# Kernel optimization log

Hardware: AMD Instinct MI355X
Metric: run time of the kernel (lower is better)

The kernel has to match this reference:

```python
import jax, jax.numpy as jnp
import numpy as np

IN_C = 1
BASE_C = 16
N3, N2, N1 = 262144, 65536, 16384

def _quadconv(feat, neigh, w, b):
    # feat: [N, C]; neigh: [N, 9] with -1 padding -> gather via extra zero row
    N = feat.shape[0]
    feat_p = jnp.concatenate([feat, jnp.zeros((1, feat.shape[1]), feat.dtype)], axis=0)
    gidx = jnp.where(neigh == -1, N, neigh)
    col = feat_p[gidx].reshape(N, -1)  # [N, 9*C] im2col
    return col @ w.T + b

def _parent_idx(keys, parent_keys):
    return jnp.searchsorted(parent_keys, keys >> 2)

def _quadpool(feat, keys, parent_keys):
    pidx = _parent_idx(keys, parent_keys)
    p = jax.ops.segment_max(feat, pidx, num_segments=parent_keys.shape[0])
    # original inits with -1e9 and zeroes untouched slots; segment_max uses -inf fill
    return jnp.where(jnp.isneginf(p), jnp.zeros((), feat.dtype), p), pidx

def _quadunpool(feat, keys, parent_keys):
    return feat[_parent_idx(keys, parent_keys)]

def _lin(key, out_f, in_f, scale=0.05):
    kw, kb = jax.random.split(key)
    return (jax.random.normal(kw, (out_f, in_f), jnp.float32) * scale,
            jnp.zeros((out_f,), jnp.float32))

def setup_inputs() -> dict:
    key = jax.random.key(0)
    ks = jax.random.split(key, 12)
    inp = {
        'features': jax.random.normal(ks[0], (N3, IN_C), jnp.float32),
        'keys3': jnp.arange(N3, dtype=jnp.int32),
        'keys2': jnp.arange(N2, dtype=jnp.int32),
        'keys1': jnp.arange(N1, dtype=jnp.int32),
        'neighs3': jax.random.randint(ks[1], (N3, 9), -1, N3, jnp.int32),
        'neighs2': jax.random.randint(ks[2], (N2, 9), -1, N2, jnp.int32),
        'neighs1': jax.random.randint(ks[3], (N1, 9), -1, N1, jnp.int32),
    }
    c = BASE_C
    inp['w_enc1'], inp['b_enc1'] = _lin(ks[4], c, 9 * IN_C)
    inp['w_enc2'], inp['b_enc2'] = _lin(ks[5], 2 * c, 9 * c)
    inp['w_enc3'], inp['b_enc3'] = _lin(ks[6], 4 * c, 9 * 2 * c)
    inp['w_dec1'], inp['b_dec1'] = _lin(ks[7], 2 * c, 9 * 4 * c)
    inp['w_dec2'], inp['b_dec2'] = _lin(ks[8], c, 9 * 2 * c)
    inp['w_head'], inp['b_head'] = _lin(ks[9], IN_C, 9 * c)
    return inp

def reference(features, keys3, keys2, keys1, neighs3, neighs2, neighs1,
              w_enc1, b_enc1, w_enc2, b_enc2, w_enc3, b_enc3,
              w_dec1, b_dec1, w_dec2, b_dec2, w_head, b_head):
    relu = jax.nn.relu
    x8 = relu(_quadconv(features, neighs3, w_enc1, b_enc1))
    x7_p, _ = _quadpool(x8, keys3, keys2)
    x7 = relu(_quadconv(x7_p, neighs2, w_enc2, b_enc2))
    x6_p, _ = _quadpool(x7, keys2, keys1)
    x6 = relu(_quadconv(x6_p, neighs1, w_enc3, b_enc3))
    x7_up = _quadunpool(x6, keys2, keys1)
    x7_dec = relu(_quadconv(x7_up, neighs2, w_dec1, b_dec1))
    x8_up = _quadunpool(x7_dec, keys3, keys2)
    x8_dec = relu(_quadconv(x8_up, neighs3, w_dec2, b_dec2))
    return _quadconv(x8_dec, neighs3, w_head, b_head)
```

## Files before the change

kernel.cpp:

```cpp
#include <hip/hip_runtime.h>
#include <stdint.h>

#define NN3 262144
#define NN2 65536
#define NN1 16384

typedef __attribute__((ext_vector_type(8))) __bf16 bf16x8;
typedef __attribute__((ext_vector_type(4))) float floatx4;

static __device__ __forceinline__ float bf2f(unsigned short u) {
    union { unsigned int i; float f; } v; v.i = ((unsigned int)u) << 16; return v.f;
}
static __device__ __forceinline__ unsigned short f2bf(float f) {
    union { float f; unsigned int i; } v; v.f = f;
    unsigned int x = v.i;
    return (unsigned short)((x + 0x7fffu + ((x >> 16) & 1u)) >> 16);
}
static __device__ __forceinline__ bf16x8 zero_bf16x8() {
    bf16x8 z;
#pragma unroll
    for (int i = 0; i < 8; ++i) z[i] = (__bf16)0.0f;
    return z;
}

__global__ __launch_bounds__(256) void enc1pool_kernel(
    const float* __restrict__ feat, const int* __restrict__ neigh,
    const float* __restrict__ w, const float* __restrict__ b,
    unsigned short* __restrict__ x7p,
    const float* __restrict__ w_enc2, const float* __restrict__ w_enc3,
    const float* __restrict__ w_dec1, const float* __restrict__ w_dec2,
    unsigned short* __restrict__ wb_enc2, unsigned short* __restrict__ wb_enc3,
    unsigned short* __restrict__ wb_dec1, unsigned short* __restrict__ wb_dec2)
{
    {
        int g = blockIdx.x * 256 + threadIdx.x;
        if (g < 4608) wb_enc2[g] = f2bf(w_enc2[g]);
        else {
            g -= 4608;
            if (g < 18432) wb_enc3[g] = f2bf(w_enc3[g]);
            else {
                g -= 18432;
                if (g < 18432) wb_dec1[g] = f2bf(w_dec1[g]);
                else { g -= 18432; if (g < 4608) wb_dec2[g] = f2bf(w_dec2[g]); }
            }
        }
    }
    __shared__ float ws[144];
    __shared__ float bs[16];
    __shared__ int nsh[2304];
    int t = threadIdx.x;
    if (t < 144) ws[t] = w[t];
    if (t < 16)  bs[t] = b[t];
    int base = blockIdx.x * 256;
    for (int e = t; e < 2304; e += 256)
        nsh[e] = __builtin_nontemporal_load(&neigh[(size_t)base * 9 + e]);
    __syncthreads();
    float f[9];
#pragma unroll
    for (int k = 0; k < 9; ++k) { int j = nsh[t * 9 + k]; f[k] = (j < 0) ? 0.0f : feat[j]; }
    float v[16];
#pragma unroll
    for (int co = 0; co < 16; ++co) {
        float a = bs[co];
#pragma unroll
        for (int k = 0; k < 9; ++k) a += f[k] * ws[co * 9 + k];
        v[co] = fmaxf(a, 0.0f);
    }
#pragma unroll
    for (int co = 0; co < 16; ++co) {
        v[co] = fmaxf(v[co], __shfl_xor(v[co], 1));
        v[co] = fmaxf(v[co], __shfl_xor(v[co], 2));
    }
    if ((t & 3) == 0) {
        unsigned int ov[8];
#pragma unroll
        for (int h = 0; h < 8; ++h)
            ov[h] = (unsigned int)f2bf(v[2 * h]) | (((unsigned int)f2bf(v[2 * h + 1])) << 16);
        uint4* dst = (uint4*)(x7p + (size_t)((base + t) >> 2) * 16);
        dst[0] = make_uint4(ov[0], ov[1], ov[2], ov[3]);
        dst[1] = make_uint4(ov[4], ov[5], ov[6], ov[7]);
    }
}

template <int CIN, int COUT, bool SHIFT, bool POOL, int TILES>
__global__ __launch_bounds__(256) void conv_mfma(
    const unsigned short* __restrict__ src, const int* __restrict__ neigh,
    const unsigned short* __restrict__ wb, const float* __restrict__ bias,
    unsigned short* __restrict__ dst)
{
    constexpr int K  = 9 * CIN;
    constexpr int KT = (K + 31) / 32;
    constexpr int NT = COUT / 16;
    __shared__ int nsh[576 * TILES];
    int t = threadIdx.x;
    int rowbase = blockIdx.x * (64 * TILES);
    for (int e = t; e < 576 * TILES; e += 256) {
        int j = __builtin_nontemporal_load(&neigh[(size_t)rowbase * 9 + e]);
        if (SHIFT) j = (j < 0) ? -1 : (j >> 2);
        nsh[e] = j;
    }
    __syncthreads();
    int lane = t & 63;
    int wave = t >> 6;
    int m    = lane & 15;
    int quad = lane >> 4;
    int mrow9 = (wave * 16 + m) * 9;
    floatx4 acc[TILES][NT];
#pragma unroll
    for (int tl = 0; tl < TILES; ++tl)
#pragma unroll
        for (int n = 0; n < NT; ++n) acc[tl][n] = (floatx4){0.f, 0.f, 0.f, 0.f};
    for (int kt = 0; kt < KT; ++kt) {
        int k0 = kt * 32 + quad * 8;
        bf16x8 a[TILES];
#pragma unroll
        for (int tl = 0; tl < TILES; ++tl) {
            a[tl] = zero_bf16x8();
            if (k0 < K) {
                int nb = k0 / CIN;
                int ci = k0 % CIN;
                int j  = nsh[tl * 576 + mrow9 + nb];
                if (j >= 0) a[tl] = *(const bf16x8*)(src + (size_t)j * CIN + ci);
            }
        }
#pragma unroll
        for (int n = 0; n < NT; ++n) {
            bf16x8 bfrag = zero_bf16x8();
            if (k0 < K) bfrag = *(const bf16x8*)(wb + (size_t)(n * 16 + m) * K + k0);
#pragma unroll
            for (int tl = 0; tl < TILES; ++tl)
                acc[tl][n] = __builtin_amdgcn_mfma_f32_16x16x32_bf16(a[tl], bfrag, acc[tl][n], 0, 0, 0);
        }
    }
#pragma unroll
    for (int tl = 0; tl < TILES; ++tl) {
        int tbase = rowbase + tl * 64;
        if (POOL) {
            int p = (tbase >> 2) + wave * 4 + quad;
#pragma unroll
            for (int n = 0; n < NT; ++n) {
                int cout = n * 16 + m;
                float vm = fmaxf(fmaxf(acc[tl][n][0], acc[tl][n][1]), fmaxf(acc[tl][n][2], acc[tl][n][3]));
                float v  = fmaxf(vm + bias[cout], 0.0f);
                dst[(size_t)p * COUT + cout] = f2bf(v);
            }
        } else {
            int grow = tbase + wave * 16 + quad * 4;
#pragma unroll
            for (int n = 0; n < NT; ++n) {
                int cout = n * 16 + m;
                float bv = bias[cout];
#pragma unroll
                for (int r = 0; r < 4; ++r) {
                    float v = fmaxf(acc[tl][n][r] + bv, 0.0f);
                    dst[(size_t)(grow + r) * COUT + cout] = f2bf(v);
                }
            }
        }
    }
}

static __device__ __forceinline__ float dot2(unsigned int u, const float* w) {
    return bf2f((unsigned short)(u & 0xffffu)) * w[0] + bf2f((unsigned short)(u >> 16)) * w[1];
}
__global__ __launch_bounds__(256) void head_kernel(
    const unsigned short* __restrict__ x, const int* __restrict__ neigh,
    const float* __restrict__ w, const float* __restrict__ b, float* __restrict__ out)
{
    __shared__ float ws[144];
    __shared__ int nsh[4608];
    int t = threadIdx.x;
    if (t < 144) ws[t] = w[t];
    int base = blockIdx.x * 512;
    for (int e = t; e < 4608; e += 256)
        nsh[e] = __builtin_nontemporal_load(&neigh[(size_t)base * 9 + e]);
    __syncthreads();
    float acc0 = b[0], acc1 = b[0];
#pragma unroll
    for (int k = 0; k < 9; ++k) {
        int j0 = nsh[t * 9 + k];
        int j1 = nsh[(256 + t) * 9 + k];
        const float* wp = &ws[k * 16];
        if (j0 >= 0) {
            const uint4* r = (const uint4*)(x + (size_t)j0 * 16);
            uint4 r0 = r[0], r1 = r[1];
            acc0 += dot2(r0.x, wp)     + dot2(r0.y, wp + 2)  + dot2(r0.z, wp + 4)  + dot2(r0.w, wp + 6);
            acc0 += dot2(r1.x, wp + 8) + dot2(r1.y, wp + 10) + dot2(r1.z, wp + 12) + dot2(r1.w, wp + 14);
        }
        if (j1 >= 0) {
            const uint4* r = (const uint4*)(x + (size_t)j1 * 16);
            uint4 r0 = r[0], r1 = r[1];
            acc1 += dot2(r0.x, wp)     + dot2(r0.y, wp + 2)  + dot2(r0.z, wp + 4)  + dot2(r0.w, wp + 6);
            acc1 += dot2(r1.x, wp + 8) + dot2(r1.y, wp + 10) + dot2(r1.z, wp + 12) + dot2(r1.w, wp + 14);
        }
    }
    __builtin_nontemporal_store(acc0, &out[base + t]);
    __builtin_nontemporal_store(acc1, &out[base + 256 + t]);
}

extern "C" void kernel_launch(void* const* d_in, const int* in_sizes, int n_in,
                              void* d_out, int out_size, void* d_ws, size_t ws_size,
                              hipStream_t stream) {
    const float* features = (const float*)d_in[0];
    const int* neighs3 = (const int*)d_in[4];
    const int* neighs2 = (const int*)d_in[5];
    const int* neighs1 = (const int*)d_in[6];
    const float* w_enc1 = (const float*)d_in[7];
    const float* b_enc1 = (const float*)d_in[8];
    const float* w_enc2 = (const float*)d_in[9];
    const float* b_enc2 = (const float*)d_in[10];
    const float* w_enc3 = (const float*)d_in[11];
    const float* b_enc3 = (const float*)d_in[12];
    const float* w_dec1 = (const float*)d_in[13];
    const float* b_dec1 = (const float*)d_in[14];
    const float* w_dec2 = (const float*)d_in[15];
    const float* b_dec2 = (const float*)d_in[16];
    const float* w_head = (const float*)d_in[17];
    const float* b_head = (const float*)d_in[18];

    char* ws = (char*)d_ws;
    size_t off = 0;
    unsigned short* wb_enc2 = (unsigned short*)(ws + off); off += 4608 * 2;
    unsigned short* wb_enc3 = (unsigned short*)(ws + off); off += 18432 * 2;
    unsigned short* wb_dec1 = (unsigned short*)(ws + off); off += 18432 * 2;
    unsigned short* wb_dec2 = (unsigned short*)(ws + off); off += 4608 * 2;
    unsigned short* x7p   = (unsigned short*)(ws + off); off += (size_t)NN2 * 16 * 2;
    unsigned short* x6p   = (unsigned short*)(ws + off); off += (size_t)NN1 * 32 * 2;
    unsigned short* x6    = (unsigned short*)(ws + off); off += (size_t)NN1 * 64 * 2;
    unsigned short* x7dec = (unsigned short*)(ws + off); off += (size_t)NN2 * 32 * 2;
    unsigned short* x8dec = (unsigned short*)(ws + off); off += (size_t)NN3 * 16 * 2;

    enc1pool_kernel<<<NN3 / 256, 256, 0, stream>>>(features, neighs3, w_enc1, b_enc1, x7p,
                                                   w_enc2, w_enc3, w_dec1, w_dec2,
                                                   wb_enc2, wb_enc3, wb_dec1, wb_dec2);
    conv_mfma<16, 32, false, true, 2><<<NN2 / 128, 256, 0, stream>>>(x7p, neighs2, wb_enc2, b_enc2, x6p);
    conv_mfma<32, 64, false, false, 1><<<NN1 / 64, 256, 0, stream>>>(x6p, neighs1, wb_enc3, b_enc3, x6);
    conv_mfma<64, 32, true, false, 2><<<NN2 / 128, 256, 0, stream>>>(x6, neighs2, wb_dec1, b_dec1, x7dec);
    conv_mfma<32, 16, true, false, 4><<<NN3 / 256, 256, 0, stream>>>(x7dec, neighs3, wb_dec2, b_dec2, x8dec);
    head_kernel<<<NN3 / 512, 256, 0, stream>>>(x8dec, neighs3, w_head, b_head, (float*)d_out);
}
```

Baseline: 202.2 us.

## Replace block-wide barriers with per-wave LDS staging and nontemporal stores

Each wave now stages its own slice of neighbor indices (and weights) in a private LDS region and syncs with a wave barrier instead of __syncthreads, so waves can start gathering without waiting on the whole block. Conv and pool outputs switch to nontemporal stores, and the head kernel's row loads go from two 16-byte loads to four 8-byte loads. This costs duplicated weight copies in LDS per wave, and the nontemporal stores may hurt later kernels that reread these activations from cache.

```diff
diff --git a/kernel.cpp b/kernel.cpp
--- a/kernel.cpp
+++ b/kernel.cpp
@@ -7,6 +7,7 @@
 
 typedef __attribute__((ext_vector_type(8))) __bf16 bf16x8;
 typedef __attribute__((ext_vector_type(4))) float floatx4;
+typedef __attribute__((ext_vector_type(4))) unsigned int uint4v;
 
 static __device__ __forceinline__ float bf2f(unsigned short u) {
     union { unsigned int i; float f; } v; v.i = ((unsigned int)u) << 16; return v.f;
@@ -45,25 +46,24 @@
             }
         }
     }
-    __shared__ float ws[144];
-    __shared__ float bs[16];
-    __shared__ int nsh[2304];
+    __shared__ float wsf[4][160];
+    __shared__ int nsh[4][576];
     int t = threadIdx.x;
-    if (t < 144) ws[t] = w[t];
-    if (t < 16)  bs[t] = b[t];
-    int base = blockIdx.x * 256;
-    for (int e = t; e < 2304; e += 256)
-        nsh[e] = __builtin_nontemporal_load(&neigh[(size_t)base * 9 + e]);
-    __syncthreads();
+    int lane = t & 63, wave = t >> 6;
+    int wbase = blockIdx.x * 256 + wave * 64;
+    for (int e = lane; e < 160; e += 64) wsf[wave][e] = (e < 144) ? w[e] : b[e - 144];
+    for (int e = lane; e < 576; e += 64)
+        nsh[wave][e] = __builtin_nontemporal_load(&neigh[(size_t)wbase * 9 + e]);
+    __builtin_amdgcn_wave_barrier();
     float f[9];
 #pragma unroll
-    for (int k = 0; k < 9; ++k) { int j = nsh[t * 9 + k]; f[k] = (j < 0) ? 0.0f : feat[j]; }
+    for (int k = 0; k < 9; ++k) { int j = nsh[wave][lane * 9 + k]; f[k] = (j < 0) ? 0.0f : feat[j]; }
     float v[16];
 #pragma unroll
     for (int co = 0; co < 16; ++co) {
-        float a = bs[co];
-#pragma unroll
-        for (int k = 0; k < 9; ++k) a += f[k] * ws[co * 9 + k];
+        float a = wsf[wave][144 + co];
+#pragma unroll
+        for (int k = 0; k < 9; ++k) a += f[k] * wsf[wave][co * 9 + k];
         v[co] = fmaxf(a, 0.0f);
     }
 #pragma unroll
@@ -71,14 +71,17 @@
         v[co] = fmaxf(v[co], __shfl_xor(v[co], 1));
         v[co] = fmaxf(v[co], __shfl_xor(v[co], 2));
     }
-    if ((t & 3) == 0) {
-        unsigned int ov[8];
-#pragma unroll
-        for (int h = 0; h < 8; ++h)
-            ov[h] = (unsigned int)f2bf(v[2 * h]) | (((unsigned int)f2bf(v[2 * h + 1])) << 16);
-        uint4* dst = (uint4*)(x7p + (size_t)((base + t) >> 2) * 16);
-        dst[0] = make_uint4(ov[0], ov[1], ov[2], ov[3]);
-        dst[1] = make_uint4(ov[4], ov[5], ov[6], ov[7]);
+    if ((lane & 3) == 0) {
+        uint4v o0, o1;
+#pragma unroll
+        for (int h = 0; h < 4; ++h)
+            o0[h] = (unsigned int)f2bf(v[2 * h]) | (((unsigned int)f2bf(v[2 * h + 1])) << 16);
+#pragma unroll
+        for (int h = 0; h < 4; ++h)
+            o1[h] = (unsigned int)f2bf(v[8 + 2 * h]) | (((unsigned int)f2bf(v[9 + 2 * h])) << 16);
+        uint4v* dst = (uint4v*)(x7p + (size_t)((wbase + lane) >> 2) * 16);
+        __builtin_nontemporal_store(o0, &dst[0]);
+        __builtin_nontemporal_store(o1, &dst[1]);
     }
 }
 
@@ -91,20 +94,22 @@
     constexpr int K  = 9 * CIN;
     constexpr int KT = (K + 31) / 32;
     constexpr int NT = COUT / 16;
-    __shared__ int nsh[576 * TILES];
+    __shared__ int nsh[4][TILES * 144];
     int t = threadIdx.x;
+    int lane = t & 63, wave = t >> 6;
     int rowbase = blockIdx.x * (64 * TILES);
-    for (int e = t; e < 576 * TILES; e += 256) {
-        int j = __builtin_nontemporal_load(&neigh[(size_t)rowbase * 9 + e]);
-        if (SHIFT) j = (j < 0) ? -1 : (j >> 2);
-        nsh[e] = j;
-    }
-    __syncthreads();
-    int lane = t & 63;
-    int wave = t >> 6;
+#pragma unroll
+    for (int tl = 0; tl < TILES; ++tl) {
+        const int* srcn = &neigh[(size_t)(rowbase + tl * 64 + wave * 16) * 9];
+        for (int e = lane; e < 144; e += 64) {
+            int j = __builtin_nontemporal_load(&srcn[e]);
+            if (SHIFT) j = (j < 0) ? -1 : (j >> 2);
+            nsh[wave][tl * 144 + e] = j;
+        }
+    }
+    __builtin_amdgcn_wave_barrier();
     int m    = lane & 15;
     int quad = lane >> 4;
-    int mrow9 = (wave * 16 + m) * 9;
     floatx4 acc[TILES][NT];
 #pragma unroll
     for (int tl = 0; tl < TILES; ++tl)
@@ -119,7 +124,7 @@
             if (k0 < K) {
                 int nb = k0 / CIN;
                 int ci = k0 % CIN;
-                int j  = nsh[tl * 576 + mrow9 + nb];
+                int j  = nsh[wave][tl * 144 + m * 9 + nb];
                 if (j >= 0) a[tl] = *(const bf16x8*)(src + (size_t)j * CIN + ci);
             }
         }
@@ -142,7 +147,7 @@
                 int cout = n * 16 + m;
                 float vm = fmaxf(fmaxf(acc[tl][n][0], acc[tl][n][1]), fmaxf(acc[tl][n][2], acc[tl][n][3]));
                 float v  = fmaxf(vm + bias[cout], 0.0f);
-                dst[(size_t)p * COUT + cout] = f2bf(v);
+                __builtin_nontemporal_store(f2bf(v), &dst[(size_t)p * COUT + cout]);
             }
         } else {
             int grow = tbase + wave * 16 + quad * 4;
@@ -153,7 +158,7 @@
 #pragma unroll
                 for (int r = 0; r < 4; ++r) {
                     float v = fmaxf(acc[tl][n][r] + bv, 0.0f);
-                    dst[(size_t)(grow + r) * COUT + cout] = f2bf(v);
+                    __builtin_nontemporal_store(f2bf(v), &dst[(size_t)(grow + r) * COUT + cout]);
                 }
             }
         }
@@ -167,35 +172,40 @@
     const unsigned short* __restrict__ x, const int* __restrict__ neigh,
     const float* __restrict__ w, const float* __restrict__ b, float* __restrict__ out)
 {
-    __shared__ float ws[144];
-    __shared__ int nsh[4608];
+    __shared__ float wsf[4][144];
+    __shared__ int nsh[4][1152];
     int t = threadIdx.x;
-    if (t < 144) ws[t] = w[t];
+    int lane = t & 63, wave = t >> 6;
     int base = blockIdx.x * 512;
-    for (int e = t; e < 4608; e += 256)
-        nsh[e] = __builtin_nontemporal_load(&neigh[(size_t)base * 9 + e]);
-    __syncthreads();
+    int r0base = base + wave * 64;
+    int r1base = base + 256 + wave * 64;
+    for (int e = lane; e < 144; e += 64) wsf[wave][e] = w[e];
+    for (int e = lane; e < 576; e += 64) {
+        nsh[wave][e]       = __builtin_nontemporal_load(&neigh[(size_t)r0base * 9 + e]);
+        nsh[wave][576 + e] = __builtin_nontemporal_load(&neigh[(size_t)r1base * 9 + e]);
+    }
+    __builtin_amdgcn_wave_barrier();
     float acc0 = b[0], acc1 = b[0];
 #pragma unroll
     for (int k = 0; k < 9; ++k) {
-        int j0 = nsh[t * 9 + k];
-        int j1 = nsh[(256 + t) * 9 + k];
-        const float* wp = &ws[k * 16];
+        int j0 = nsh[wave][lane * 9 + k];
+        int j1 = nsh[wave][576 + lane * 9 + k];
+        const float* wp = &wsf[wave][k * 16];
         if (j0 >= 0) {
-            const uint4* r = (const uint4*)(x + (size_t)j0 * 16);
-            uint4 r0 = r[0], r1 = r[1];
-            acc0 += dot2(r0.x, wp)     + dot2(r0.y, wp + 2)  + dot2(r0.z, wp + 4)  + dot2(r0.w, wp + 6);
-            acc0 += dot2(r1.x, wp + 8) + dot2(r1.y, wp + 10) + dot2(r1.z, wp + 12) + dot2(r1.w, wp + 14);
+            const uint2* r = (const uint2*)(x + (size_t)j0 * 16);
+            uint2 a = r[0], c = r[1], d = r[2], e2 = r[3];
+            acc0 += dot2(a.x, wp)      + dot2(a.y, wp + 2)  + dot2(c.x, wp + 4)  + dot2(c.y, wp + 6);
+            acc0 += dot2(d.x, wp + 8)  + dot2(d.y, wp + 10) + dot2(e2.x, wp + 12) + dot2(e2.y, wp + 14);
         }
         if (j1 >= 0) {
-            const uint4* r = (const uint4*)(x + (size_t)j1 * 16);
-            uint4 r0 = r[0], r1 = r[1];
-            acc1 += dot2(r0.x, wp)     + dot2(r0.y, wp + 2)  + dot2(r0.z, wp + 4)  + dot2(r0.w, wp + 6);
-            acc1 += dot2(r1.x, wp + 8) + dot2(r1.y, wp + 10) + dot2(r1.z, wp + 12) + dot2(r1.w, wp + 14);
-        }
-    }
-    __builtin_nontemporal_store(acc0, &out[base + t]);
-    __builtin_nontemporal_store(acc1, &out[base + 256 + t]);
+            const uint2* r = (const uint2*)(x + (size_t)j1 * 16);
+            uint2 a = r[0], c = r[1], d = r[2], e2 = r[3];
+            acc1 += dot2(a.x, wp)      + dot2(a.y, wp + 2)  + dot2(c.x, wp + 4)  + dot2(c.y, wp + 6);
+            acc1 += dot2(d.x, wp + 8)  + dot2(d.y, wp + 10) + dot2(e2.x, wp + 12) + dot2(e2.y, wp + 14);
+        }
+    }
+    __builtin_nontemporal_store(acc0, &out[r0base + lane]);
+    __builtin_nontemporal_store(acc1, &out[r1base + lane]);
 }
 
 extern "C" void kernel_launch(void* const* d_in, const int* in_sizes, int n_in,
```

Result: no change. 202.6 us (+0.2%).
